# Kernel optimization log

Measured on AMD Instinct MI355X. Metric: run time of the kernel, lower is better.

Reference implementation:

```python
import jax, jax.numpy as jnp
import numpy as np

B, BEAM, V, L = 32, 5, 128000, 512
PAD_IDX, EOS_IDX = 0, 2


def setup_inputs() -> dict:
    key = jax.random.key(0)
    k1, k2 = jax.random.split(key, 2)
    # decoder log-prob output for current step, one row per (sentence, beam)
    scores = jax.nn.log_softmax(
        jax.random.normal(k1, (B * BEAM, V), dtype=jnp.float32), axis=-1)
    # beam 0 active, others at -inf (as in _generate init)
    beam_scores = jnp.concatenate(
        [jnp.zeros((B, 1), jnp.float32),
         jnp.full((B, BEAM - 1), -1e9, jnp.float32)], axis=1)
    generated = jax.random.randint(k2, (B * BEAM, L), 4, V).astype(jnp.int32)
    return {"scores": scores, "beam_scores": beam_scores,
            "generated": generated, "cur_len": 256}


def reference(scores, beam_scores, generated, cur_len):
    # combined scores: [B*BEAM, V] + [B*BEAM, 1] -> view as [B, BEAM*V]
    comb = (scores + beam_scores.reshape(-1, 1)).reshape(B, BEAM * V)
    # topk 2*beam candidates per sentence (sorted descending, like torch.topk)
    next_scores, next_words = jax.lax.top_k(comb, 2 * BEAM)  # [B, 2*BEAM]
    beam_id = next_words // V
    word_id = next_words % V
    # eos candidates go to hypotheses list; keep first BEAM non-eos candidates
    non_eos = word_id != EOS_IDX
    # stable sort preserves descending-score order among non-eos entries
    order = jnp.argsort(jnp.where(non_eos, 0, 1), axis=1, stable=True)[:, :BEAM]
    sel_scores = jnp.take_along_axis(next_scores, order, axis=1)  # [B, BEAM]
    sel_words = jnp.take_along_axis(word_id, order, axis=1)
    sel_beam = jnp.take_along_axis(beam_id, order, axis=1)
    sel_valid = jnpp_valid = jnp.take_along_axis(non_eos, order, axis=1)
    # fallback slots (fewer than BEAM non-eos): (score=0, word=pad, beam=0)
    sel_scores = jnp.where(sel_valid, sel_scores, 0.0)
    sel_words = jnp.where(sel_valid, sel_words, PAD_IDX).astype(generated.dtype)
    eff_beam = jnp.where(
        sel_valid, jnp.arange(B)[:, None] * BEAM + sel_beam, 0).reshape(-1)
    # reorder hypotheses and append new words at column cur_len
    new_generated = generated[eff_beam].at[:, cur_len].set(sel_words.reshape(-1))
    return new_generated, sel_scores
```

## Files before the change

### kernel.cpp

```cpp
#include <hip/hip_runtime.h>
#include <math.h>

#define B        32
#define BEAM     5
#define V        128000
#define L        512
#define PAD_IDX  0
#define EOS_IDX  2
#define NROWS    (B * BEAM)
#define TOPK     10

#define CHUNK4   4096
#define ROW4     (V / 4)
#define CPR      8
#define FULL_IT  (CHUNK4 / 256)
#define TAIL4    (ROW4 - (CPR - 1) * CHUNK4)
#define TAIL_IT  (TAIL4 / 256)
#define NBLK1    (NROWS * CPR)
#define P1WAVES  4
#define CAND_PER_SENT (BEAM * CPR * P1WAVES * TOPK)
#define NCAND    (B * CAND_PER_SENT)
#define WS_NEED  ((size_t)NCAND * 8)

#define SENT_I   0x7FFFFFFF

__device__ __forceinline__ void insert10(float v, int idx,
                                         float (&ts)[TOPK], int (&ti)[TOPK]) {
    if (!((v > ts[TOPK - 1]) || (v == ts[TOPK - 1] && idx < ti[TOPK - 1]))) return;
    float cv = v; int ci = idx;
#pragma unroll
    for (int j = 0; j < TOPK; ++j) {
        bool gt = (cv > ts[j]) || (cv == ts[j] && ci < ti[j]);
        float tv = ts[j]; int tj = ti[j];
        if (gt) { ts[j] = cv; ti[j] = ci; cv = tv; ci = tj; }
    }
}

__device__ __forceinline__ int decode_len(const int* p) {
    int v = p[0];
    if ((unsigned)v < (unsigned)L) return v;
    float f = __int_as_float(v);
    int fi_ = (int)f;
    if (f == (float)fi_ && (unsigned)fi_ < (unsigned)L) return fi_;
    return v & (L - 1);
}

__global__ __launch_bounds__(256) void p1_scan_topk(
    const float* __restrict__ scores,
    const float* __restrict__ beam_scores,
    float* __restrict__ cand_s,
    int*   __restrict__ cand_i)
{
    const int bid   = blockIdx.x;
    const int row   = bid >> 3;
    const int chunk = bid & 7;
    const int beam  = row % BEAM;

    const float4* p = (const float4*)(scores + (size_t)row * V)
                      + chunk * CHUNK4 + threadIdx.x;
    const int e0 = (chunk * CHUNK4 + (int)threadIdx.x) * 4;

    float ts[TOPK]; int ti[TOPK];
#pragma unroll
    for (int j = 0; j < TOPK; ++j) { ts[j] = -INFINITY; ti[j] = SENT_I; }

    const int iters = (chunk == CPR - 1) ? TAIL_IT : FULL_IT;
    for (int it = 0; it < iters; ++it) {
        float4 f = p[it * 256];
        float m = fmaxf(fmaxf(f.x, f.y), fmaxf(f.z, f.w));
        if (m >= ts[TOPK - 1]) {
            int e = e0 + it * 1024;
            insert10(f.x, e,     ts, ti);
            insert10(f.y, e + 1, ts, ti);
            insert10(f.z, e + 2, ts, ti);
            insert10(f.w, e + 3, ts, ti);
        }
    }

    const int lane    = threadIdx.x & 63;
    const int waveid  = threadIdx.x >> 6;
    const int outbase = (bid * P1WAVES + waveid) * TOPK;
    const float bs    = beam_scores[row];
    const int idx_base = beam * V;

    for (int k = 0; k < TOPK; ++k) {
        float v = ts[0]; int idx = ti[0]; int who = lane;
#pragma unroll
        for (int off = 1; off < 64; off <<= 1) {
            float ov = __shfl_xor(v, off);
            int   oi = __shfl_xor(idx, off);
            int   ow = __shfl_xor(who, off);
            if ((ov > v) || (ov == v && oi < idx)) { v = ov; idx = oi; who = ow; }
        }
        if (lane == 0) {
            cand_s[outbase + k] = v + bs;
            cand_i[outbase + k] = idx_base + idx;
        }
        if (lane == who) {
#pragma unroll
            for (int j = 0; j < TOPK - 1; ++j) { ts[j] = ts[j + 1]; ti[j] = ti[j + 1]; }
            ts[TOPK - 1] = -INFINITY; ti[TOPK - 1] = SENT_I;
        }
    }
}

__global__ __launch_bounds__(256) void p2_merge_select(
    const float* __restrict__ cand_s,
    const int*   __restrict__ cand_i,
    const int*   __restrict__ generated,
    const int*   __restrict__ cur_len_p,
    float* __restrict__ out_f32)
{
    const int b   = blockIdx.x;
    const int tid = threadIdx.x;

    __shared__ float fs[TOPK];
    __shared__ int   fi[TOPK];
    __shared__ int   sh_word[BEAM], sh_src[BEAM];
    __shared__ int   sh_cur;

    if (tid < 64) {
        float ts[TOPK]; int ti[TOPK];
#pragma unroll
        for (int j = 0; j < TOPK; ++j) { ts[j] = -INFINITY; ti[j] = SENT_I; }

        const float* cs = cand_s + b * CAND_PER_SENT;
        const int*   ci = cand_i + b * CAND_PER_SENT;
#pragma unroll
        for (int i = 0; i < CAND_PER_SENT / 64; ++i)
            insert10(cs[tid + 64 * i], ci[tid + 64 * i], ts, ti);

        for (int k = 0; k < TOPK; ++k) {
            float v = ts[0]; int idx = ti[0]; int who = tid;
#pragma unroll
            for (int off = 1; off < 64; off <<= 1) {
                float ov = __shfl_xor(v, off);
                int   oi = __shfl_xor(idx, off);
                int   ow = __shfl_xor(who, off);
                if ((ov > v) || (ov == v && oi < idx)) { v = ov; idx = oi; who = ow; }
            }
            if (tid == 0) { fs[k] = v; fi[k] = idx; }
            if (tid == who) {
#pragma unroll
                for (int j = 0; j < TOPK - 1; ++j) { ts[j] = ts[j + 1]; ti[j] = ti[j + 1]; }
                ts[TOPK - 1] = -INFINITY; ti[TOPK - 1] = SENT_I;
            }
        }

        if (tid == 0) {
            sh_cur = decode_len(cur_len_p);
            int cnt = 0;
            for (int k = 0; k < TOPK && cnt < BEAM; ++k) {
                int idx  = fi[k];
                int bm   = idx / V;
                int word = idx - bm * V;
                if (word != EOS_IDX) {
                    sh_word[cnt] = word;
                    sh_src[cnt]  = b * BEAM + bm;
                    out_f32[NROWS * L + b * BEAM + cnt] = fs[k];
                    ++cnt;
                }
            }
            for (; cnt < BEAM; ++cnt) {
                sh_word[cnt] = PAD_IDX;
                sh_src[cnt]  = 0;
                out_f32[NROWS * L + b * BEAM + cnt] = 0.0f;
            }
        }
    }
    __syncthreads();

    const int cur = sh_cur;
    for (int i = tid; i < BEAM * L; i += 256) {
        int slot = i >> 9;
        int col  = i & (L - 1);
        int val  = (col == cur) ? sh_word[slot]
                                : generated[sh_src[slot] * L + col];
        out_f32[(b * BEAM + slot) * L + col] = (float)val;
    }
}

__global__ __launch_bounds__(1024) void beam_step_fb(
    const float* __restrict__ scores,
    const float* __restrict__ beam_scores,
    const int*   __restrict__ generated,
    const int*   __restrict__ cur_len_p,
    float* __restrict__ out_f32)
{
    const int b    = blockIdx.x;
    const int tid  = threadIdx.x;
    const int lane = tid & 63;
    const int wave = tid >> 6;

    __shared__ float cs[16 * TOPK];
    __shared__ int   ci[16 * TOPK];
    __shared__ float fs[TOPK];
    __shared__ int   fi[TOPK];
    __shared__ int   sh_word[BEAM], sh_src[BEAM];
    __shared__ int   sh_cur;

    float ts[TOPK]; int ti[TOPK];
#pragma unroll
    for (int j = 0; j < TOPK; ++j) { ts[j] = -INFINITY; ti[j] = SENT_I; }

    for (int beam = 0; beam < BEAM; ++beam) {
        const float   bs = beam_scores[b * BEAM + beam];
        const float4* p  = (const float4*)(scores + (size_t)(b * BEAM + beam) * V);
        const int     ib = beam * V;
        for (int j4 = tid; j4 < ROW4; j4 += 1024) {
            float4 f = p[j4];
            float x = f.x + bs, y = f.y + bs, z = f.z + bs, w = f.w + bs;
            float m = fmaxf(fmaxf(x, y), fmaxf(z, w));
            if (m >= ts[TOPK - 1]) {
                int e = ib + j4 * 4;
                insert10(x, e, ts, ti); insert10(y, e + 1, ts, ti);
                insert10(z, e + 2, ts, ti); insert10(w, e + 3, ts, ti);
            }
        }
    }
    for (int k = 0; k < TOPK; ++k) {
        float v = ts[0]; int idx = ti[0]; int who = lane;
#pragma unroll
        for (int off = 1; off < 64; off <<= 1) {
            float ov = __shfl_xor(v, off); int oi = __shfl_xor(idx, off);
            int ow = __shfl_xor(who, off);
            if ((ov > v) || (ov == v && oi < idx)) { v = ov; idx = oi; who = ow; }
        }
        if (lane == 0) { cs[wave * TOPK + k] = v; ci[wave * TOPK + k] = idx; }
        if (lane == who) {
#pragma unroll
            for (int j = 0; j < TOPK - 1; ++j) { ts[j] = ts[j + 1]; ti[j] = ti[j + 1]; }
            ts[TOPK - 1] = -INFINITY; ti[TOPK - 1] = SENT_I;
        }
    }
    __syncthreads();
    if (wave == 0) {
#pragma unroll
        for (int j = 0; j < TOPK; ++j) { ts[j] = -INFINITY; ti[j] = SENT_I; }
        for (int i = lane; i < 16 * TOPK; i += 64) insert10(cs[i], ci[i], ts, ti);
        for (int k = 0; k < TOPK; ++k) {
            float v = ts[0]; int idx = ti[0]; int who = lane;
#pragma unroll
            for (int off = 1; off < 64; off <<= 1) {
                float ov = __shfl_xor(v, off); int oi = __shfl_xor(idx, off);
                int ow = __shfl_xor(who, off);
                if ((ov > v) || (ov == v && oi < idx)) { v = ov; idx = oi; who = ow; }
            }
            if (lane == 0) { fs[k] = v; fi[k] = idx; }
            if (lane == who) {
#pragma unroll
                for (int j = 0; j < TOPK - 1; ++j) { ts[j] = ts[j + 1]; ti[j] = ti[j + 1]; }
                ts[TOPK - 1] = -INFINITY; ti[TOPK - 1] = SENT_I;
            }
        }
        if (lane == 0) {
            sh_cur = decode_len(cur_len_p);
            int cnt = 0;
            for (int k = 0; k < TOPK && cnt < BEAM; ++k) {
                int idx = fi[k]; int bm = idx / V; int word = idx - bm * V;
                if (word != EOS_IDX) {
                    sh_word[cnt] = word; sh_src[cnt] = b * BEAM + bm;
                    out_f32[NROWS * L + b * BEAM + cnt] = fs[k];
                    ++cnt;
                }
            }
            for (; cnt < BEAM; ++cnt) {
                sh_word[cnt] = PAD_IDX; sh_src[cnt] = 0;
                out_f32[NROWS * L + b * BEAM + cnt] = 0.0f;
            }
        }
    }
    __syncthreads();
    const int cur = sh_cur;
    for (int i = tid; i < BEAM * L; i += 1024) {
        int slot = i >> 9; int col = i & (L - 1);
        int val = (col == cur) ? sh_word[slot]
                               : generated[sh_src[slot] * L + col];
        out_f32[(b * BEAM + slot) * L + col] = (float)val;
    }
}

extern "C" void kernel_launch(void* const* d_in, const int* in_sizes, int n_in,
                              void* d_out, int out_size, void* d_ws, size_t ws_size,
                              hipStream_t stream) {
    const float* scores      = nullptr;
    const float* beam_scores = nullptr;
    const int*   generated   = nullptr;
    const int*   cur_len_p   = nullptr;
    for (int i = 0; i < n_in; ++i) {
        switch (in_sizes[i]) {
            case NROWS * V:  scores      = (const float*)d_in[i]; break;
            case NROWS:      beam_scores = (const float*)d_in[i]; break;
            case NROWS * L:  generated   = (const int*)d_in[i];   break;
            case 1:          cur_len_p   = (const int*)d_in[i];   break;
            default: break;
        }
    }
    if (!scores)      scores      = (const float*)d_in[0];
    if (!beam_scores) beam_scores = (const float*)d_in[1];
    if (!generated)   generated   = (const int*)d_in[2];
    if (!cur_len_p)   cur_len_p   = (const int*)d_in[3];

    float* out_f32 = (float*)d_out;

    if (ws_size >= WS_NEED) {
        float* cand_s = (float*)d_ws;
        int*   cand_i = (int*)((float*)d_ws + NCAND);
        p1_scan_topk<<<NBLK1, 256, 0, stream>>>(scores, beam_scores, cand_s, cand_i);
        p2_merge_select<<<B, 256, 0, stream>>>(cand_s, cand_i, generated, cur_len_p,
                                               out_f32);
    } else {
        beam_step_fb<<<B, 1024, 0, stream>>>(scores, beam_scores, generated,
                                             cur_len_p, out_f32);
    }
}
```

Measured before the change: 234.5 us.

## Add sampled threshold pre-pass to prune top-k insertions in scan

Adds a first kernel that samples the first 4096 elements of each beam row per sentence and takes the 10th-largest combined score as a per-sentence threshold. The main scan then skips insertion work for any float4 whose max plus beam score falls below that threshold, and it adds the beam score and beam offset in the scan rather than afterwards. The merge kernel now spreads candidate reading across all four waves and the shuffle reductions drop the owner-lane tracking. The cost is an extra kernel launch and a second read of the sampled prefix, in exchange for less insertion-sort work in the scan.

```diff
diff --git a/kernel.cpp b/kernel.cpp
--- a/kernel.cpp
+++ b/kernel.cpp
@@ -20,9 +20,13 @@
 #define P1WAVES  4
 #define CAND_PER_SENT (BEAM * CPR * P1WAVES * TOPK)
 #define NCAND    (B * CAND_PER_SENT)
-#define WS_NEED  ((size_t)NCAND * 8)
+
+#define SAMP4    1024
+
+#define WS_NEED  (256 + (size_t)NCAND * 8)
 
 #define SENT_I   0x7FFFFFFF
+
 
 __device__ __forceinline__ void insert10(float v, int idx,
                                          float (&ts)[TOPK], int (&ti)[TOPK]) {
@@ -34,6 +38,30 @@
         float tv = ts[j]; int tj = ti[j];
         if (gt) { ts[j] = cv; ti[j] = ci; cv = tv; ci = tj; }
     }
+}
+
+__device__ __forceinline__ void popPair(float (&ts)[TOPK], int (&ti)[TOPK]) {
+#pragma unroll
+    for (int j = 0; j < TOPK - 1; ++j) { ts[j] = ts[j + 1]; ti[j] = ti[j + 1]; }
+    ts[TOPK - 1] = -INFINITY; ti[TOPK - 1] = SENT_I;
+}
+
+__device__ __forceinline__ void insV(float v, float (&ts)[TOPK]) {
+    if (v < ts[TOPK - 1]) return;
+    float cv = v;
+#pragma unroll
+    for (int j = 0; j < TOPK; ++j) {
+        float t = ts[j];
+        bool ge = (cv >= t);
+        ts[j] = ge ? cv : t;
+        cv    = ge ? t : cv;
+    }
+}
+
+__device__ __forceinline__ void popVal(float (&ts)[TOPK]) {
+#pragma unroll
+    for (int j = 0; j < TOPK - 1; ++j) ts[j] = ts[j + 1];
+    ts[TOPK - 1] = -INFINITY;
 }
 
 __device__ __forceinline__ int decode_len(const int* p) {
@@ -45,9 +73,59 @@
     return v & (L - 1);
 }
 
-__global__ __launch_bounds__(256) void p1_scan_topk(
+__global__ __launch_bounds__(256, 4) void a_theta(
     const float* __restrict__ scores,
     const float* __restrict__ beam_scores,
+    float* __restrict__ theta)
+{
+    const int b    = blockIdx.x;
+    const int tid  = threadIdx.x;
+    const int lane = tid & 63;
+    const int wave = tid >> 6;
+
+    float ts[TOPK];
+#pragma unroll
+    for (int j = 0; j < TOPK; ++j) ts[j] = -INFINITY;
+
+    for (int r = 0; r < BEAM; ++r) {
+        const int row = b * BEAM + r;
+        const float bs = beam_scores[row];
+        const float4* p = (const float4*)(scores + (size_t)row * V);
+#pragma unroll
+        for (int it = 0; it < SAMP4 / 256; ++it) {
+            float4 f = p[it * 256 + tid];
+            insV(f.x + bs, ts); insV(f.y + bs, ts);
+            insV(f.z + bs, ts); insV(f.w + bs, ts);
+        }
+    }
+
+    __shared__ float wtop[4][TOPK];
+    for (int k = 0; k < TOPK; ++k) {
+        float v = ts[0];
+#pragma unroll
+        for (int off = 1; off < 64; off <<= 1) v = fmaxf(v, __shfl_xor(v, off));
+        if (lane == 0) wtop[wave][k] = v;
+        if (ts[0] == v) popVal(ts);
+    }
+    __syncthreads();
+    if (wave == 0) {
+        float v0 = (lane < 4 * TOPK) ? wtop[lane / TOPK][lane % TOPK] : -INFINITY;
+        float th = -INFINITY;
+        for (int k = 0; k < TOPK; ++k) {
+            float v = v0;
+#pragma unroll
+            for (int off = 1; off < 64; off <<= 1) v = fmaxf(v, __shfl_xor(v, off));
+            th = v;
+            if (v0 == v) v0 = -INFINITY;
+        }
+        if (lane == 0) theta[b] = th;
+    }
+}
+
+__global__ __launch_bounds__(256, 4) void b_scan(
+    const float* __restrict__ scores,
+    const float* __restrict__ beam_scores,
+    const float* __restrict__ theta,
     float* __restrict__ cand_s,
     int*   __restrict__ cand_i)
 {
@@ -55,10 +133,12 @@
     const int row   = bid >> 3;
     const int chunk = bid & 7;
     const int beam  = row % BEAM;
+    const float bs  = beam_scores[row];
+    const float th  = theta[row / BEAM];
 
     const float4* p = (const float4*)(scores + (size_t)row * V)
                       + chunk * CHUNK4 + threadIdx.x;
-    const int e0 = (chunk * CHUNK4 + (int)threadIdx.x) * 4;
+    const int e0 = (chunk * CHUNK4 + (int)threadIdx.x) * 4 + beam * V;
 
     float ts[TOPK]; int ti[TOPK];
 #pragma unroll
@@ -68,96 +148,110 @@
     for (int it = 0; it < iters; ++it) {
         float4 f = p[it * 256];
         float m = fmaxf(fmaxf(f.x, f.y), fmaxf(f.z, f.w));
-        if (m >= ts[TOPK - 1]) {
+        if (m + bs >= th) {
             int e = e0 + it * 1024;
-            insert10(f.x, e,     ts, ti);
-            insert10(f.y, e + 1, ts, ti);
-            insert10(f.z, e + 2, ts, ti);
-            insert10(f.w, e + 3, ts, ti);
+            insert10(f.x + bs, e,     ts, ti);
+            insert10(f.y + bs, e + 1, ts, ti);
+            insert10(f.z + bs, e + 2, ts, ti);
+            insert10(f.w + bs, e + 3, ts, ti);
         }
     }
 
     const int lane    = threadIdx.x & 63;
-    const int waveid  = threadIdx.x >> 6;
-    const int outbase = (bid * P1WAVES + waveid) * TOPK;
-    const float bs    = beam_scores[row];
-    const int idx_base = beam * V;
-
-    for (int k = 0; k < TOPK; ++k) {
-        float v = ts[0]; int idx = ti[0]; int who = lane;
+    const int wv      = threadIdx.x >> 6;
+    const int outbase = (bid * P1WAVES + wv) * TOPK;
+
+    int k = 0;
+    for (; k < TOPK; ++k) {
+        float v = ts[0]; int idx = ti[0];
 #pragma unroll
         for (int off = 1; off < 64; off <<= 1) {
             float ov = __shfl_xor(v, off);
             int   oi = __shfl_xor(idx, off);
-            int   ow = __shfl_xor(who, off);
-            if ((ov > v) || (ov == v && oi < idx)) { v = ov; idx = oi; who = ow; }
-        }
-        if (lane == 0) {
-            cand_s[outbase + k] = v + bs;
-            cand_i[outbase + k] = idx_base + idx;
-        }
-        if (lane == who) {
-#pragma unroll
-            for (int j = 0; j < TOPK - 1; ++j) { ts[j] = ts[j + 1]; ti[j] = ti[j + 1]; }
-            ts[TOPK - 1] = -INFINITY; ti[TOPK - 1] = SENT_I;
-        }
-    }
-}
-
-__global__ __launch_bounds__(256) void p2_merge_select(
+            if ((ov > v) || (ov == v && oi < idx)) { v = ov; idx = oi; }
+        }
+        if (v == -INFINITY) break;
+        if (lane == 0) { cand_s[outbase + k] = v; cand_i[outbase + k] = idx; }
+        if (ts[0] == v && ti[0] == idx) popPair(ts, ti);
+    }
+    if (lane >= k && lane < TOPK) {
+        cand_s[outbase + lane] = -INFINITY;
+        cand_i[outbase + lane] = SENT_I;
+    }
+}
+
+__global__ __launch_bounds__(256, 4) void c_select(
     const float* __restrict__ cand_s,
     const int*   __restrict__ cand_i,
     const int*   __restrict__ generated,
     const int*   __restrict__ cur_len_p,
     float* __restrict__ out_f32)
 {
-    const int b   = blockIdx.x;
-    const int tid = threadIdx.x;
-
+    const int b    = blockIdx.x;
+    const int tid  = threadIdx.x;
+    const int lane = tid & 63;
+    const int wave = tid >> 6;
+
+    __shared__ float swv[4][TOPK];
+    __shared__ int   swi[4][TOPK];
     __shared__ float fs[TOPK];
     __shared__ int   fi[TOPK];
     __shared__ int   sh_word[BEAM], sh_src[BEAM];
     __shared__ int   sh_cur;
 
-    if (tid < 64) {
-        float ts[TOPK]; int ti[TOPK];
-#pragma unroll
-        for (int j = 0; j < TOPK; ++j) { ts[j] = -INFINITY; ti[j] = SENT_I; }
-
-        const float* cs = cand_s + b * CAND_PER_SENT;
-        const int*   ci = cand_i + b * CAND_PER_SENT;
-#pragma unroll
-        for (int i = 0; i < CAND_PER_SENT / 64; ++i)
-            insert10(cs[tid + 64 * i], ci[tid + 64 * i], ts, ti);
-
-        for (int k = 0; k < TOPK; ++k) {
-            float v = ts[0]; int idx = ti[0]; int who = tid;
+    float ts[TOPK]; int ti[TOPK];
+#pragma unroll
+    for (int j = 0; j < TOPK; ++j) { ts[j] = -INFINITY; ti[j] = SENT_I; }
+
+    const int base = b * CAND_PER_SENT;
+    for (int i = tid; i < CAND_PER_SENT; i += 256)
+        insert10(cand_s[base + i], cand_i[base + i], ts, ti);
+
+    int k = 0;
+    for (; k < TOPK; ++k) {
+        float v = ts[0]; int idx = ti[0];
+#pragma unroll
+        for (int off = 1; off < 64; off <<= 1) {
+            float ov = __shfl_xor(v, off);
+            int   oi = __shfl_xor(idx, off);
+            if ((ov > v) || (ov == v && oi < idx)) { v = ov; idx = oi; }
+        }
+        if (v == -INFINITY) break;
+        if (lane == 0) { swv[wave][k] = v; swi[wave][k] = idx; }
+        if (ts[0] == v && ti[0] == idx) popPair(ts, ti);
+    }
+    if (lane >= k && lane < TOPK) {
+        swv[wave][lane] = -INFINITY; swi[wave][lane] = SENT_I;
+    }
+    __syncthreads();
+
+    if (wave == 0) {
+        float v0; int i0;
+        if (lane < 4 * TOPK) { v0 = swv[lane / TOPK][lane % TOPK];
+                               i0 = swi[lane / TOPK][lane % TOPK]; }
+        else                 { v0 = -INFINITY; i0 = SENT_I; }
+        for (int r = 0; r < TOPK; ++r) {
+            float v = v0; int idx = i0;
 #pragma unroll
             for (int off = 1; off < 64; off <<= 1) {
                 float ov = __shfl_xor(v, off);
                 int   oi = __shfl_xor(idx, off);
-                int   ow = __shfl_xor(who, off);
-                if ((ov > v) || (ov == v && oi < idx)) { v = ov; idx = oi; who = ow; }
-            }
-            if (tid == 0) { fs[k] = v; fi[k] = idx; }
-            if (tid == who) {
-#pragma unroll
-                for (int j = 0; j < TOPK - 1; ++j) { ts[j] = ts[j + 1]; ti[j] = ti[j + 1]; }
-                ts[TOPK - 1] = -INFINITY; ti[TOPK - 1] = SENT_I;
-            }
-        }
-
-        if (tid == 0) {
+                if ((ov > v) || (ov == v && oi < idx)) { v = ov; idx = oi; }
+            }
+            if (lane == 0) { fs[r] = v; fi[r] = idx; }
+            if (v0 == v && i0 == idx) { v0 = -INFINITY; i0 = SENT_I; }
+        }
+        if (lane == 0) {
             sh_cur = decode_len(cur_len_p);
             int cnt = 0;
-            for (int k = 0; k < TOPK && cnt < BEAM; ++k) {
-                int idx  = fi[k];
+            for (int kk = 0; kk < TOPK && cnt < BEAM; ++kk) {
+                int idx  = fi[kk];
                 int bm   = idx / V;
                 int word = idx - bm * V;
                 if (word != EOS_IDX) {
                     sh_word[cnt] = word;
                     sh_src[cnt]  = b * BEAM + bm;
-                    out_f32[NROWS * L + b * BEAM + cnt] = fs[k];
+                    out_f32[NROWS * L + b * BEAM + cnt] = fs[kk];
                     ++cnt;
                 }
             }
@@ -219,19 +313,14 @@
         }
     }
     for (int k = 0; k < TOPK; ++k) {
-        float v = ts[0]; int idx = ti[0]; int who = lane;
+        float v = ts[0]; int idx = ti[0];
 #pragma unroll
         for (int off = 1; off < 64; off <<= 1) {
             float ov = __shfl_xor(v, off); int oi = __shfl_xor(idx, off);
-            int ow = __shfl_xor(who, off);
-            if ((ov > v) || (ov == v && oi < idx)) { v = ov; idx = oi; who = ow; }
+            if ((ov > v) || (ov == v && oi < idx)) { v = ov; idx = oi; }
         }
         if (lane == 0) { cs[wave * TOPK + k] = v; ci[wave * TOPK + k] = idx; }
-        if (lane == who) {
-#pragma unroll
-            for (int j = 0; j < TOPK - 1; ++j) { ts[j] = ts[j + 1]; ti[j] = ti[j + 1]; }
-            ts[TOPK - 1] = -INFINITY; ti[TOPK - 1] = SENT_I;
-        }
+        if (ts[0] == v && ti[0] == idx) popPair(ts, ti);
     }
     __syncthreads();
     if (wave == 0) {
@@ -239,19 +328,14 @@
         for (int j = 0; j < TOPK; ++j) { ts[j] = -INFINITY; ti[j] = SENT_I; }
         for (int i = lane; i < 16 * TOPK; i += 64) insert10(cs[i], ci[i], ts, ti);
         for (int k = 0; k < TOPK; ++k) {
-            float v = ts[0]; int idx = ti[0]; int who = lane;
+            float v = ts[0]; int idx = ti[0];
 #pragma unroll
             for (int off = 1; off < 64; off <<= 1) {
                 float ov = __shfl_xor(v, off); int oi = __shfl_xor(idx, off);
-                int ow = __shfl_xor(who, off);
-                if ((ov > v) || (ov == v && oi < idx)) { v = ov; idx = oi; who = ow; }
+                if ((ov > v) || (ov == v && oi < idx)) { v = ov; idx = oi; }
             }
             if (lane == 0) { fs[k] = v; fi[k] = idx; }
-            if (lane == who) {
-#pragma unroll
-                for (int j = 0; j < TOPK - 1; ++j) { ts[j] = ts[j + 1]; ti[j] = ti[j + 1]; }
-                ts[TOPK - 1] = -INFINITY; ti[TOPK - 1] = SENT_I;
-            }
+            if (ts[0] == v && ti[0] == idx) popPair(ts, ti);
         }
         if (lane == 0) {
             sh_cur = decode_len(cur_len_p);
@@ -304,11 +388,14 @@
     float* out_f32 = (float*)d_out;
 
     if (ws_size >= WS_NEED) {
-        float* cand_s = (float*)d_ws;
-        int*   cand_i = (int*)((float*)d_ws + NCAND);
-        p1_scan_topk<<<NBLK1, 256, 0, stream>>>(scores, beam_scores, cand_s, cand_i);
-        p2_merge_select<<<B, 256, 0, stream>>>(cand_s, cand_i, generated, cur_len_p,
-                                               out_f32);
+        float* theta  = (float*)d_ws;
+        float* cand_s = (float*)((char*)d_ws + 256);
+        int*   cand_i = (int*)((char*)d_ws + 256 + (size_t)NCAND * 4);
+        a_theta<<<B, 256, 0, stream>>>(scores, beam_scores, theta);
+        b_scan<<<NBLK1, 256, 0, stream>>>(scores, beam_scores, theta,
+                                          cand_s, cand_i);
+        c_select<<<B, 256, 0, stream>>>(cand_s, cand_i, generated, cur_len_p,
+                                        out_f32);
     } else {
         beam_step_fb<<<B, 1024, 0, stream>>>(scores, beam_scores, generated,
                                              cur_len_p, out_f32);
```

After: 193.0 us. 1.21x faster.
